# Kernel optimization log

Hardware: AMD Instinct MI355X
Metric: run time of the kernel (lower is better)

## Reference

```python
import jax, jax.numpy as jnp
import numpy as np

TEMP = 0.07


def setup_inputs() -> dict:
    key = jax.random.key(0)
    k1, k2 = jax.random.split(key)
    B, m, d = 256, 128, 768
    v_final = jax.random.normal(k1, (B, d), dtype=jnp.float32)
    T_fused = jax.random.normal(k2, (B, m, d), dtype=jnp.float32)
    return {"v_final": v_final, "T_fused": T_fused}


def reference(v_final, T_fused):
    B = v_final.shape[0]
    # [B, B, m] token-level similarities, scaled by temperature
    sim = jnp.einsum('id,jmd->ijm', v_final, T_fused) / TEMP
    # max over text tokens (ColBERT max-sim) -> [B, B]
    sim_max = sim.max(axis=-1)
    targets = jnp.arange(B)
    # symmetric cross-entropy with diagonal targets
    logp_i2t = jax.nn.log_softmax(sim_max, axis=-1)
    logp_t2i = jax.nn.log_softmax(sim_max.T, axis=-1)
    loss_i2t = -jnp.mean(logp_i2t[targets, targets])
    loss_t2i = -jnp.mean(logp_t2i[targets, targets])
    return (loss_i2t + loss_t2i) / 2
```

## Files before the change

### kernel.cpp

```cpp
#include <hip/hip_runtime.h>
#include <hip/hip_bf16.h>

constexpr int BATCH = 256;
constexpr int MTOK  = 128;
constexpr int DDIM  = 768;
constexpr int NV    = BATCH * DDIM;
constexpr float INV_TEMP = 1.0f / 0.07f;

typedef __bf16 bf16;
typedef __bf16 bf16x8 __attribute__((ext_vector_type(8)));
typedef float  f32x4  __attribute__((ext_vector_type(4)));

__global__ __launch_bounds__(256) void pack_v_kernel(
        const float* __restrict__ V, bf16x8* __restrict__ Vq) {
    int c = blockIdx.x * 256 + threadIdx.x;
    int lane = c & 63, fs = c >> 6;
    int ks = fs % 24, g = fs / 24;
    int l15 = lane & 15, quad = lane >> 4;
    const float* src = V + (size_t)(g * 16 + l15) * DDIM + ks * 32 + quad * 8;
    float4 f0 = *(const float4*)(src);
    float4 f1 = *(const float4*)(src + 4);
    bf16x8 o;
    o[0] = (bf16)f0.x; o[1] = (bf16)f0.y; o[2] = (bf16)f0.z; o[3] = (bf16)f0.w;
    o[4] = (bf16)f1.x; o[5] = (bf16)f1.y; o[6] = (bf16)f1.z; o[7] = (bf16)f1.w;
    Vq[c] = o;
}

__global__ __launch_bounds__(256, 2) void gemm_max_kernel(
        const bf16*  __restrict__ Vq,
        const float* __restrict__ T,
        float* __restrict__ Sp) {
    __shared__ char  ldsB[2 * 8192];
    __shared__ float smax[256];

    const int jt   = blockIdx.x >> 1;
    const int nh   = blockIdx.x & 1;
    const int tid  = threadIdx.x;
    const int w    = tid >> 6;
    const int lane = tid & 63;
    const int quad = lane >> 4;
    const int l15  = lane & 15;

    const bf16* aBase[4];
#pragma unroll
    for (int t = 0; t < 4; ++t)
        aBase[t] = Vq + ((size_t)(w * 4 + t) * 24) * 512 + lane * 8;

    const float* gB[2];
    int bwoff[2];
#pragma unroll
    for (int q = 0; q < 2; ++q) {
        int c = q * 256 + tid;
        int row = c >> 3, kp = c & 7;
        gB[q] = T + (size_t)(jt * MTOK + nh * 64 + row) * DDIM + kp * 8;
        bwoff[q] = (kp >> 2) * 4096 + row * 64 + ((kp & 3) << 4);
    }

    int boff[2][4];
#pragma unroll
    for (int h = 0; h < 2; ++h)
#pragma unroll
        for (int tc = 0; tc < 4; ++tc)
            boff[h][tc] = h * 4096 + (tc * 16 + l15) * 64 + quad * 16;

    f32x4 acc[4][4] = {};

    auto cvt_store = [&](float4 a, float4 b, int q, int bufo) {
        bf16x8 o;
        o[0] = (bf16)a.x; o[1] = (bf16)a.y; o[2] = (bf16)a.z; o[3] = (bf16)a.w;
        o[4] = (bf16)b.x; o[5] = (bf16)b.y; o[6] = (bf16)b.z; o[7] = (bf16)b.w;
        *(bf16x8*)(ldsB + bufo + bwoff[q]) = o;
    };

    float4 breg[2][2];
#pragma unroll
    for (int q = 0; q < 2; ++q) {
        float4 r0 = *(const float4*)(gB[q]);
        float4 r1 = *(const float4*)(gB[q] + 4);
        cvt_store(r0, r1, q, 0);
        breg[q][0] = *(const float4*)(gB[q] + 64);
        breg[q][1] = *(const float4*)(gB[q] + 64 + 4);
    }
    bf16x8 apre[2][4];
#pragma unroll
    for (int h = 0; h < 2; ++h)
#pragma unroll
        for (int t = 0; t < 4; ++t)
            apre[h][t] = *(const bf16x8*)(aBase[t] + (size_t)h * 512);
    __syncthreads();

    for (int kk = 0; kk < 12; ++kk) {
        const int buf  = (kk & 1) * 8192;
        const int nbuf = buf ^ 8192;
        if (kk < 11) {
#pragma unroll
            for (int q = 0; q < 2; ++q)
                cvt_store(breg[q][0], breg[q][1], q, nbuf);
        }
        if (kk < 10) {
#pragma unroll
            for (int q = 0; q < 2; ++q) {
                const float* p = gB[q] + (kk + 2) * 64;
                breg[q][0] = *(const float4*)(p);
                breg[q][1] = *(const float4*)(p + 4);
            }
        }
#pragma unroll
        for (int h = 0; h < 2; ++h) {
            const int hs = kk * 2 + h;
            bf16x8 af[4], bb[4];
#pragma unroll
            for (int t = 0; t < 4; ++t) af[t] = apre[h][t];
            if (hs + 2 < 24) {
#pragma unroll
                for (int t = 0; t < 4; ++t)
                    apre[h][t] = *(const bf16x8*)(aBase[t] + (size_t)(hs + 2) * 512);
            }
#pragma unroll
            for (int tc = 0; tc < 4; ++tc)
                bb[tc] = *(const bf16x8*)(ldsB + buf + boff[h][tc]);
#pragma unroll
            for (int tr = 0; tr < 4; ++tr)
#pragma unroll
                for (int tc = 0; tc < 4; ++tc)
                    acc[tr][tc] = __builtin_amdgcn_mfma_f32_16x16x32_bf16(
                        af[tr], bb[tc], acc[tr][tc], 0, 0, 0);
        }
        __syncthreads();
    }

#pragma unroll
    for (int tr = 0; tr < 4; ++tr) {
#pragma unroll
        for (int r = 0; r < 4; ++r) {
            float v = fmaxf(fmaxf(acc[tr][0][r], acc[tr][1][r]),
                            fmaxf(acc[tr][2][r], acc[tr][3][r]));
            v = fmaxf(v, __shfl_xor(v, 1, 64));
            v = fmaxf(v, __shfl_xor(v, 2, 64));
            v = fmaxf(v, __shfl_xor(v, 4, 64));
            v = fmaxf(v, __shfl_xor(v, 8, 64));
            if (l15 == 0)
                smax[w * 64 + tr * 16 + quad * 4 + r] = v;
        }
    }
    __syncthreads();
    Sp[((size_t)nh * BATCH + jt) * BATCH + tid] = smax[tid] * INV_TEMP;
}

__global__ __launch_bounds__(64) void ce1_kernel(
        const float* __restrict__ Sp, float* __restrict__ partial) {
    const int t = blockIdx.x;
    const int l = threadIdx.x;
    const float* Sp0 = Sp;
    const float* Sp1 = Sp + BATCH * BATCH;

    float vr[4], vc[4];
#pragma unroll
    for (int p = 0; p < 4; ++p) {
        int j = p * 64 + l;
        vr[p] = fmaxf(Sp0[j * BATCH + t], Sp1[j * BATCH + t]);
        int i = p * 64 + l;
        vc[p] = fmaxf(Sp0[t * BATCH + i], Sp1[t * BATCH + i]);
    }
    float mr = fmaxf(fmaxf(vr[0], vr[1]), fmaxf(vr[2], vr[3]));
    float mc = fmaxf(fmaxf(vc[0], vc[1]), fmaxf(vc[2], vc[3]));
    for (int o = 32; o > 0; o >>= 1) {
        mr = fmaxf(mr, __shfl_xor(mr, o, 64));
        mc = fmaxf(mc, __shfl_xor(mc, o, 64));
    }
    float sr = 0.f, sc = 0.f;
#pragma unroll
    for (int p = 0; p < 4; ++p) {
        sr += expf(vr[p] - mr);
        sc += expf(vc[p] - mc);
    }
    for (int o = 32; o > 0; o >>= 1) {
        sr += __shfl_xor(sr, o, 64);
        sc += __shfl_xor(sc, o, 64);
    }
    if (l == 0) {
        float diag = fmaxf(Sp0[t * BATCH + t], Sp1[t * BATCH + t]);
        partial[t] = 0.5f * ((mr + logf(sr)) + (mc + logf(sc))) - diag;
    }
}

__global__ __launch_bounds__(256) void ce2_kernel(
        const float* __restrict__ partial, float* __restrict__ out) {
    const int i = threadIdx.x;
    float term = partial[i];
    for (int o = 32; o > 0; o >>= 1) term += __shfl_down(term, o, 64);
    __shared__ float ps[4];
    if ((i & 63) == 0) ps[i >> 6] = term;
    __syncthreads();
    if (i == 0) out[0] = (ps[0] + ps[1] + ps[2] + ps[3]) / (float)BATCH;
}

extern "C" void kernel_launch(void* const* d_in, const int* in_sizes, int n_in,
                              void* d_out, int out_size, void* d_ws, size_t ws_size,
                              hipStream_t stream) {
    const float* v = (const float*)d_in[0];
    const float* T = (const float*)d_in[1];

    bf16*  Vq = (bf16*)d_ws;
    float* Sp = (float*)((char*)d_ws + (size_t)NV * sizeof(bf16));
    float* partial = Sp + 2 * BATCH * BATCH;

    pack_v_kernel<<<96, 256, 0, stream>>>(v, (bf16x8*)Vq);
    gemm_max_kernel<<<512, 256, 0, stream>>>(Vq, T, Sp);
    ce1_kernel<<<256, 64, 0, stream>>>(Sp, partial);
    ce2_kernel<<<1, 256, 0, stream>>>(partial, (float*)d_out);
}
```

Measured before the change: 163.9 us.

## Double k-chunk size per sync in GEMM and fuse final CE reduction

The GEMM main loop now stages two 64-wide k-slices of T per LDS buffer (32 KB double buffer), halving the number of loop iterations and __syncthreads barriers. Global prefetch of T is deepened to match. Separately, the two cross-entropy kernels are merged: each block atomically bumps a counter (reset in pack_v) and the last block performs the final sum, removing one kernel launch. The larger LDS footprint and extra prefetch registers may reduce occupancy at the 2-block launch bound.

Measured after the change: 168.1 us. 2.6% more time.

```diff
diff --git a/kernel.cpp b/kernel.cpp
--- a/kernel.cpp
+++ b/kernel.cpp
@@ -12,7 +12,9 @@
 typedef float  f32x4  __attribute__((ext_vector_type(4)));
 
 __global__ __launch_bounds__(256) void pack_v_kernel(
-        const float* __restrict__ V, bf16x8* __restrict__ Vq) {
+        const float* __restrict__ V, bf16x8* __restrict__ Vq,
+        unsigned int* __restrict__ counter) {
+    if (blockIdx.x == 0 && threadIdx.x == 0) *counter = 0u;
     int c = blockIdx.x * 256 + threadIdx.x;
     int lane = c & 63, fs = c >> 6;
     int ks = fs % 24, g = fs / 24;
@@ -30,7 +32,7 @@
         const bf16*  __restrict__ Vq,
         const float* __restrict__ T,
         float* __restrict__ Sp) {
-    __shared__ char  ldsB[2 * 8192];
+    __shared__ char  ldsB[2 * 16384];
     __shared__ float smax[256];
 
     const int jt   = blockIdx.x >> 1;
@@ -55,13 +57,7 @@
         gB[q] = T + (size_t)(jt * MTOK + nh * 64 + row) * DDIM + kp * 8;
         bwoff[q] = (kp >> 2) * 4096 + row * 64 + ((kp & 3) << 4);
     }
-
-    int boff[2][4];
-#pragma unroll
-    for (int h = 0; h < 2; ++h)
-#pragma unroll
-        for (int tc = 0; tc < 4; ++tc)
-            boff[h][tc] = h * 4096 + (tc * 16 + l15) * 64 + quad * 16;
+    const int brd = l15 * 64 + quad * 16;
 
     f32x4 acc[4][4] = {};
 
@@ -72,53 +68,61 @@
         *(bf16x8*)(ldsB + bufo + bwoff[q]) = o;
     };
 
-    float4 breg[2][2];
-#pragma unroll
-    for (int q = 0; q < 2; ++q) {
-        float4 r0 = *(const float4*)(gB[q]);
-        float4 r1 = *(const float4*)(gB[q] + 4);
-        cvt_store(r0, r1, q, 0);
-        breg[q][0] = *(const float4*)(gB[q] + 64);
-        breg[q][1] = *(const float4*)(gB[q] + 64 + 4);
-    }
+    float4 breg[2][2][2];
+#pragma unroll
+    for (int q = 0; q < 2; ++q)
+#pragma unroll
+        for (int s = 0; s < 2; ++s) {
+            const float* p = gB[q] + s * 64;
+            float4 r0 = *(const float4*)(p);
+            float4 r1 = *(const float4*)(p + 4);
+            cvt_store(r0, r1, q, s * 8192);
+            breg[q][s][0] = *(const float4*)(p + 128);
+            breg[q][s][1] = *(const float4*)(p + 128 + 4);
+        }
     bf16x8 apre[2][4];
 #pragma unroll
-    for (int h = 0; h < 2; ++h)
+    for (int hp = 0; hp < 2; ++hp)
 #pragma unroll
         for (int t = 0; t < 4; ++t)
-            apre[h][t] = *(const bf16x8*)(aBase[t] + (size_t)h * 512);
+            apre[hp][t] = *(const bf16x8*)(aBase[t] + (size_t)hp * 512);
     __syncthreads();
 
-    for (int kk = 0; kk < 12; ++kk) {
-        const int buf  = (kk & 1) * 8192;
-        const int nbuf = buf ^ 8192;
-        if (kk < 11) {
+    for (int kk = 0; kk < 6; ++kk) {
+        const int buf  = (kk & 1) * 16384;
+        const int nbuf = buf ^ 16384;
+        if (kk < 5) {
 #pragma unroll
             for (int q = 0; q < 2; ++q)
-                cvt_store(breg[q][0], breg[q][1], q, nbuf);
-        }
-        if (kk < 10) {
-#pragma unroll
-            for (int q = 0; q < 2; ++q) {
-                const float* p = gB[q] + (kk + 2) * 64;
-                breg[q][0] = *(const float4*)(p);
-                breg[q][1] = *(const float4*)(p + 4);
+#pragma unroll
+                for (int s = 0; s < 2; ++s)
+                    cvt_store(breg[q][s][0], breg[q][s][1], q, nbuf + s * 8192);
+        }
+        if (kk < 4) {
+#pragma unroll
+            for (int q = 0; q < 2; ++q)
+#pragma unroll
+                for (int s = 0; s < 2; ++s) {
+                    const float* p = gB[q] + (2 * kk + 4 + s) * 64;
+                    breg[q][s][0] = *(const float4*)(p);
+                    breg[q][s][1] = *(const float4*)(p + 4);
+                }
+        }
+#pragma unroll
+        for (int h = 0; h < 4; ++h) {
+            const int hs = kk * 4 + h;
+            bf16x8 af[4], bb[4];
+#pragma unroll
+            for (int t = 0; t < 4; ++t) af[t] = apre[h & 1][t];
+            if (hs + 2 < 24) {
+#pragma unroll
+                for (int t = 0; t < 4; ++t)
+                    apre[h & 1][t] = *(const bf16x8*)(aBase[t] + (size_t)(hs + 2) * 512);
             }
-        }
-#pragma unroll
-        for (int h = 0; h < 2; ++h) {
-            const int hs = kk * 2 + h;
-            bf16x8 af[4], bb[4];
-#pragma unroll
-            for (int t = 0; t < 4; ++t) af[t] = apre[h][t];
-            if (hs + 2 < 24) {
-#pragma unroll
-                for (int t = 0; t < 4; ++t)
-                    apre[h][t] = *(const bf16x8*)(aBase[t] + (size_t)(hs + 2) * 512);
-            }
+            const int hb = buf + (h >> 1) * 8192 + (h & 1) * 4096;
 #pragma unroll
             for (int tc = 0; tc < 4; ++tc)
-                bb[tc] = *(const bf16x8*)(ldsB + buf + boff[h][tc]);
+                bb[tc] = *(const bf16x8*)(ldsB + hb + tc * 1024 + brd);
 #pragma unroll
             for (int tr = 0; tr < 4; ++tr)
 #pragma unroll
@@ -147,8 +151,9 @@
     Sp[((size_t)nh * BATCH + jt) * BATCH + tid] = smax[tid] * INV_TEMP;
 }
 
-__global__ __launch_bounds__(64) void ce1_kernel(
-        const float* __restrict__ Sp, float* __restrict__ partial) {
+__global__ __launch_bounds__(64) void ce_kernel(
+        const float* __restrict__ Sp, float* __restrict__ partial,
+        unsigned int* __restrict__ counter, float* __restrict__ out) {
     const int t = blockIdx.x;
     const int l = threadIdx.x;
     const float* Sp0 = Sp;
@@ -159,8 +164,7 @@
     for (int p = 0; p < 4; ++p) {
         int j = p * 64 + l;
         vr[p] = fmaxf(Sp0[j * BATCH + t], Sp1[j * BATCH + t]);
-        int i = p * 64 + l;
-        vc[p] = fmaxf(Sp0[t * BATCH + i], Sp1[t * BATCH + i]);
+        vc[p] = fmaxf(Sp0[t * BATCH + j], Sp1[t * BATCH + j]);
     }
     float mr = fmaxf(fmaxf(vr[0], vr[1]), fmaxf(vr[2], vr[3]));
     float mc = fmaxf(fmaxf(vc[0], vc[1]), fmaxf(vc[2], vc[3]));
@@ -178,21 +182,21 @@
         sr += __shfl_xor(sr, o, 64);
         sc += __shfl_xor(sc, o, 64);
     }
+    __shared__ int isLast;
     if (l == 0) {
         float diag = fmaxf(Sp0[t * BATCH + t], Sp1[t * BATCH + t]);
         partial[t] = 0.5f * ((mr + logf(sr)) + (mc + logf(sc))) - diag;
-    }
-}
-
-__global__ __launch_bounds__(256) void ce2_kernel(
-        const float* __restrict__ partial, float* __restrict__ out) {
-    const int i = threadIdx.x;
-    float term = partial[i];
-    for (int o = 32; o > 0; o >>= 1) term += __shfl_down(term, o, 64);
-    __shared__ float ps[4];
-    if ((i & 63) == 0) ps[i >> 6] = term;
+        __threadfence();
+        unsigned int old = atomicAdd(counter, 1u);
+        isLast = (old == (unsigned int)(BATCH - 1));
+    }
     __syncthreads();
-    if (i == 0) out[0] = (ps[0] + ps[1] + ps[2] + ps[3]) / (float)BATCH;
+    if (isLast) {
+        __threadfence();
+        float s = partial[l] + partial[l + 64] + partial[l + 128] + partial[l + 192];
+        for (int o = 32; o > 0; o >>= 1) s += __shfl_xor(s, o, 64);
+        if (l == 0) out[0] = s / (float)BATCH;
+    }
 }
 
 extern "C" void kernel_launch(void* const* d_in, const int* in_sizes, int n_in,
@@ -204,9 +208,9 @@
     bf16*  Vq = (bf16*)d_ws;
     float* Sp = (float*)((char*)d_ws + (size_t)NV * sizeof(bf16));
     float* partial = Sp + 2 * BATCH * BATCH;
-
-    pack_v_kernel<<<96, 256, 0, stream>>>(v, (bf16x8*)Vq);
+    unsigned int* counter = (unsigned int*)(partial + BATCH);
+
+    pack_v_kernel<<<96, 256, 0, stream>>>(v, (bf16x8*)Vq, counter);
     gemm_max_kernel<<<512, 256, 0, stream>>>(Vq, T, Sp);
-    ce1_kernel<<<256, 64, 0, stream>>>(Sp, partial);
-    ce2_kernel<<<1, 256, 0, stream>>>(partial, (float*)d_out);
-}
+    ce_kernel<<<256, 64, 0, stream>>>(Sp, partial, counter, (float*)d_out);
+}
```
